# Optimization experiments

Measured on AMD Instinct MI355X. Metric: run time of the kernel, lower is better.

The kernel has to match this reference:

```python
import jax, jax.numpy as jnp
import numpy as np

NUM_GROUPS = 32
EPS = 1e-6
NUM_HEADS = 8


def group_norm32(x, gamma, beta):
    # GroupNorm32: compute in float32, cast back to input dtype.
    b, c, h, w = x.shape
    xf = x.astype(jnp.float32).reshape(b, NUM_GROUPS, -1)  # [b, G, (C/G)*h*w]
    mean = xf.mean(axis=-1, keepdims=True)
    var = xf.var(axis=-1, keepdims=True)
    xn = ((xf - mean) * jax.lax.rsqrt(var + EPS)).reshape(b, c, h, w)
    xn = xn * gamma[None, :, None, None] + beta[None, :, None, None]
    return xn.astype(x.dtype)


def setup_inputs() -> dict:
    key = jax.random.key(0)
    ks = jax.random.split(key, 4)
    b, c, h, w = 16, 512, 32, 32
    x = jax.random.normal(ks[0], (b, c, h, w), dtype=jnp.float32)
    w_qkv = jax.random.normal(ks[1], (3 * c, c), dtype=jnp.float32) * (1.0 / np.sqrt(c))
    b_qkv = jnp.zeros((3 * c,), dtype=jnp.float32)
    w_proj = jax.random.normal(ks[2], (c, c), dtype=jnp.float32) * (1.0 / np.sqrt(c))
    b_proj = jnp.zeros((c,), dtype=jnp.float32)
    gamma = jnp.ones((c,), dtype=jnp.float32)
    beta = jnp.zeros((c,), dtype=jnp.float32)
    return {"x": x, "w_qkv": w_qkv, "b_qkv": b_qkv, "w_proj": w_proj,
            "b_proj": b_proj, "gamma": gamma, "beta": beta}


def reference(x, w_qkv, b_qkv, w_proj, b_proj, gamma, beta):
    b, c, h, w = x.shape
    H = NUM_HEADS
    d = c // H
    n = h * w
    x_norm = group_norm32(x, gamma, beta)
    # 1x1 conv == channel matmul
    qkv = jnp.einsum('oc,bchw->bohw', w_qkv, x_norm) + b_qkv[None, :, None, None]
    q, k, v = jnp.split(qkv, 3, axis=1)
    q = q.reshape(b, H, d, n)
    k = k.reshape(b, H, d, n)
    v = v.reshape(b, H, d, n)
    scale = d ** (-0.5)
    attn = jnp.einsum('bhdn,bhdm->bhnm', q, k) * scale  # [b,H,n,n]
    attn = jax.nn.softmax(attn, axis=-1)
    out = jnp.einsum('bhnm,bhdm->bhdn', attn, v).reshape(b, c, h, w)
    proj = jnp.einsum('oc,bchw->bohw', w_proj, out) + b_proj[None, :, None, None]
    return x + proj
```

## Files before the change

### kernel.cpp

```cpp
#include <hip/hip_runtime.h>
#include <hip/hip_bf16.h>

typedef __bf16 bf16;
typedef __bf16 bf16x4 __attribute__((ext_vector_type(4)));
typedef __bf16 bf16x8 __attribute__((ext_vector_type(8)));
typedef float  floatx4 __attribute__((ext_vector_type(4)));
typedef float  f32x16  __attribute__((ext_vector_type(16)));

#define BB   16
#define CC   512
#define NN   1024
#define GG   32
#define CPG  16
#define HH   8
#define DD   64
#define QSCALE 0.18033688011f

#if __has_builtin(__builtin_amdgcn_exp2f)
#define EXP2(x) __builtin_amdgcn_exp2f(x)
#else
#define EXP2(x) exp2f(x)
#endif

__device__ inline floatx4 mfma16(bf16x8 a, bf16x8 b, floatx4 c) {
    return __builtin_amdgcn_mfma_f32_16x16x32_bf16(a, b, c, 0, 0, 0);
}
__device__ inline f32x16 mfma32(bf16x8 a, bf16x8 b, f32x16 c) {
    return __builtin_amdgcn_mfma_f32_32x32x16_bf16(a, b, c, 0, 0, 0);
}

__device__ inline floatx4 zero4() {
    floatx4 z; z[0] = 0.f; z[1] = 0.f; z[2] = 0.f; z[3] = 0.f; return z;
}

__device__ inline void gl_lds16(const bf16* g, bf16* l) {
    __builtin_amdgcn_global_load_lds(
        (const __attribute__((address_space(1))) unsigned int*)g,
        (__attribute__((address_space(3))) unsigned int*)l, 16, 0, 0);
}

__device__ inline unsigned cvt_pk_bf16(float a, float b) {
    unsigned r;
    asm("v_cvt_pk_bf16_f32 %0, %1, %2" : "=v"(r) : "v"(a), "v"(b));
    return r;
}
__device__ inline void pl32swap(unsigned &x, unsigned &y) {
    asm volatile("v_permlane32_swap_b32 %0, %1" : "+v"(x), "+v"(y));
}

__device__ inline float ldf(const void* p, size_t i, int isb) {
    return isb ? (float)((const bf16*)p)[i] : ((const float*)p)[i];
}
__device__ inline floatx4 ldf4(const void* p, size_t i, int isb) {
    floatx4 o;
    if (isb) {
        bf16x4 v = *(const bf16x4*)((const bf16*)p + i);
        #pragma unroll
        for (int j = 0; j < 4; ++j) o[j] = (float)v[j];
    } else {
        o = *(const floatx4*)((const float*)p + i);
    }
    return o;
}
__device__ inline void stf(void* p, size_t i, float v, int isb) {
    if (isb) ((bf16*)p)[i] = (bf16)v; else ((float*)p)[i] = v;
}

__global__ __launch_bounds__(256) void flag_kernel(const void* x, const void* wq,
        const void* wp, const void* gamma, int* flags) {
    __shared__ int bad[3];
    const int tid = threadIdx.x;
    if (tid < 3) bad[tid] = 0;
    __syncthreads();
    const void* arrs[3] = {x, wq, wp};
    #pragma unroll
    for (int a = 0; a < 3; ++a) {
        const unsigned short* u = (const unsigned short*)arrs[a];
        int c = 0;
        for (int i = tid * 32; i < tid * 32 + 32; ++i) {
            if ((u[i] & 0x7F80) == 0x7F80) c = 1;
        }
        if (c) atomicOr(&bad[a], 1);
    }
    __syncthreads();
    if (tid == 0) {
        flags[0] = bad[0] ? 0 : 1;
        flags[1] = bad[1] ? 0 : 1;
        flags[2] = bad[2] ? 0 : 1;
        flags[3] = (((const unsigned short*)gamma)[0] == 0x3F80) ? 1 : 0;
    }
}

__global__ __launch_bounds__(256) void cvt_kernel(const void* __restrict__ src,
        bf16* __restrict__ dst, int n, const int* __restrict__ flags, int fidx) {
    const int f = flags[fidx];
    int i = (blockIdx.x * 256 + threadIdx.x) * 4;
    if (i >= n) return;
    if (f) {
        *(bf16x4*)(dst + i) = *(const bf16x4*)((const bf16*)src + i);
    } else {
        const float* s = (const float*)src + i;
        bf16x4 o;
        #pragma unroll
        for (int j = 0; j < 4; ++j) o[j] = (bf16)s[j];
        *(bf16x4*)(dst + i) = o;
    }
}

__global__ __launch_bounds__(256) void gn_kernel(const void* __restrict__ x,
        const void* __restrict__ gamma, const void* __restrict__ beta,
        bf16* __restrict__ xn_t, const int* __restrict__ flags, int b0) {
    const int fx = flags[0], fg = flags[3];
    const int bg = blockIdx.x;
    const int bl = bg >> 5, g = bg & 31;
    const int tid = threadIdx.x;
    const size_t xbase = (size_t)((b0 + bl) * CC + g * CPG) * NN;

    float s = 0.f, ss = 0.f;
    for (int i = tid * 4; i < CPG * NN; i += 1024) {
        floatx4 v = ldf4(x, xbase + i, fx);
        #pragma unroll
        for (int j = 0; j < 4; ++j) { s += v[j]; ss += v[j] * v[j]; }
    }
    for (int off = 32; off > 0; off >>= 1) {
        s  += __shfl_down(s, off);
        ss += __shfl_down(ss, off);
    }
    __shared__ float red[8];
    __shared__ float stats[2];
    const int wave = tid >> 6;
    if ((tid & 63) == 0) { red[wave] = s; red[4 + wave] = ss; }
    __syncthreads();
    if (tid == 0) {
        float S  = red[0] + red[1] + red[2] + red[3];
        float SS = red[4] + red[5] + red[6] + red[7];
        float mean = S * (1.0f / (CPG * NN));
        float var  = SS * (1.0f / (CPG * NN)) - mean * mean;
        stats[0] = mean;
        stats[1] = rsqrtf(fmaxf(var, 0.f) + 1e-6f);
    }
    __syncthreads();
    const float mean = stats[0], rstd = stats[1];

    __shared__ __align__(16) float tile[CPG][64];
    const int cn = tid >> 4;
    const int nb = (tid & 15) * 4;
    const float gm1 = ldf(gamma, g * CPG + cn, fg);
    const float bt1 = ldf(beta,  g * CPG + cn, fg);
    const int n2 = tid >> 2, cq = tid & 3;
    for (int nt = 0; nt < NN / 64; ++nt) {
        floatx4 v = ldf4(x, xbase + (size_t)cn * NN + nt * 64 + nb, fx);
        #pragma unroll
        for (int j = 0; j < 4; ++j)
            tile[cn][nb + j] = (v[j] - mean) * rstd * gm1 + bt1;
        __syncthreads();
        bf16x4 o;
        #pragma unroll
        for (int k = 0; k < 4; ++k) o[k] = (bf16)tile[cq * 4 + k][n2];
        *(bf16x4*)(xn_t + (size_t)(bl * NN + nt * 64 + n2) * CC + g * CPG + cq * 4) = o;
        __syncthreads();
    }
}

__global__ __launch_bounds__(256) void qkv_kernel(const bf16* __restrict__ wq_b,
        const bf16* __restrict__ b_qkv, const bf16* __restrict__ xn_t,
        bf16* __restrict__ q_t, bf16* __restrict__ k_pk, bf16* __restrict__ v_pk) {
    __shared__ __align__(16) bf16 As[2][128 * 32];
    __shared__ __align__(16) bf16 Bs[2][128 * 32];

    const int ntile = blockIdx.x;
    const int mtile = blockIdx.y;
    const int bl = blockIdx.z;
    const int w = threadIdx.x >> 6, lane = threadIdx.x & 63;
    const int l16 = lane & 15, quad = lane >> 4;
    const int wr = w >> 1, wc = w & 1;

    const int mbase = mtile * 128, nbase = ntile * 128;
    const int srow = lane >> 2;
    const int scol = (((lane & 3) ^ ((srow >> 1) & 3)) << 3);
    const bf16* Ag = wq_b + (size_t)(mbase + w * 32 + srow) * CC + scol;
    const bf16* Bg = xn_t + (size_t)bl * NN * CC + (size_t)(nbase + w * 32 + srow) * CC + scol;
    const int ldso = (2 * w) * 512;

#define QSTAGE(buf, k0) do {                                  \
    gl_lds16(Ag + (k0),           &As[buf][ldso]);            \
    gl_lds16(Ag + 16 * CC + (k0), &As[buf][ldso + 512]);      \
    gl_lds16(Bg + (k0),           &Bs[buf][ldso]);            \
    gl_lds16(Bg + 16 * CC + (k0), &Bs[buf][ldso + 512]);      \
} while (0)

    floatx4 acc[4][4];
    #pragma unroll
    for (int i = 0; i < 4; ++i)
        #pragma unroll
        for (int j = 0; j < 4; ++j) acc[i][j] = zero4();

    const int sw = (l16 >> 1) & 3;
    QSTAGE(0, 0);

    for (int it = 0; it < 16; ++it) {
        const int cur = it & 1;
        const int nk = ((it + 1) & 15) * 32;
        QSTAGE(cur ^ 1, nk);
        asm volatile("s_waitcnt vmcnt(4)" ::: "memory");
        __builtin_amdgcn_s_barrier();

        bf16x8 af[4], bfr[4];
        #pragma unroll
        for (int mt = 0; mt < 4; ++mt)
            af[mt] = *(const bf16x8*)&As[cur][(wr * 64 + mt * 16 + l16) * 32 + ((quad ^ sw) << 3)];
        #pragma unroll
        for (int nt = 0; nt < 4; ++nt)
            bfr[nt] = *(const bf16x8*)&Bs[cur][(wc * 64 + nt * 16 + l16) * 32 + ((quad ^ sw) << 3)];

        asm volatile("s_waitcnt lgkmcnt(0)" ::: "memory");
        __builtin_amdgcn_s_barrier();

        #pragma unroll
        for (int mt = 0; mt < 4; ++mt)
            #pragma unroll
            for (int nt = 0; nt < 4; ++nt)
                acc[mt][nt] = mfma16(af[mt], bfr[nt], acc[mt][nt]);
    }
#undef QSTAGE

    const int qsel = mtile >> 2;
    const int obase = (mtile & 3) * 128;
    #pragma unroll
    for (int mt = 0; mt < 4; ++mt) {
        const int op = obase + wr * 64 + mt * 16 + quad * 4;
        float bias[4];
        #pragma unroll
        for (int r = 0; r < 4; ++r) bias[r] = (float)b_qkv[qsel * CC + op + r];
        #pragma unroll
        for (int nt = 0; nt < 4; ++nt) {
            const int p = nbase + wc * 64 + nt * 16 + l16;
            if (qsel == 0) {
                int h = op >> 6, d0 = op & 63;
                bf16x4 o;
                #pragma unroll
                for (int r = 0; r < 4; ++r) o[r] = (bf16)((acc[mt][nt][r] + bias[r]) * QSCALE);
                *(bf16x4*)(q_t + ((size_t)(bl * HH + h) * NN + p) * DD + d0) = o;
            } else if (qsel == 1) {
                int h = op >> 6, d0 = op & 63;
                bf16x4 o;
                #pragma unroll
                for (int r = 0; r < 4; ++r) o[r] = (bf16)(acc[mt][nt][r] + bias[r]);
                size_t off = ((size_t)(bl * HH + h) << 16) + ((size_t)(p >> 5) << 11)
                           + ((d0 >> 4) << 9) + (((d0 >> 3) & 1) << 8)
                           + ((p & 31) << 3) + (d0 & 7);
                *(bf16x4*)(k_pk + off) = o;
            } else {
                #pragma unroll
                for (int r = 0; r < 4; ++r) {
                    int c = op + r;
                    int h = c >> 6, d = c & 63;
                    size_t off = ((size_t)(bl * HH + h) << 16) + ((size_t)(p >> 4) << 10)
                               + ((d >> 5) << 9) + (((p >> 3) & 1) << 8)
                               + ((d & 31) << 3) + (p & 7);
                    v_pk[off] = (bf16)(acc[mt][nt][r] + bias[r]);
                }
            }
        }
    }
}

__global__ __launch_bounds__(256) void attn_kernel(const bf16* __restrict__ q_t,
        const bf16* __restrict__ k_pk, const bf16* __restrict__ v_pk,
        bf16* __restrict__ attn_out) {
    const int lid = blockIdx.x + (blockIdx.y << 2);
    const int xcd = lid & 7, jj = lid >> 3;
    const int bh = xcd * (gridDim.y >> 3) + (jj >> 2);
    const int qb = jj & 3;
    const int bl = bh >> 3, h = bh & 7;
    const int tid = threadIdx.x;
    const int w = tid >> 6, lane = tid & 63;
    const int l31 = lane & 31, hi = lane >> 5;

    const bf16* kpb = k_pk + ((size_t)bh << 16) + (hi << 8) + (l31 << 3);
    const bf16* vpb = v_pk + ((size_t)bh << 16) + (hi << 8) + (l31 << 3);

    const int qbase = qb * 256 + w * 64;
    const bf16* qp = q_t + ((size_t)bh * NN + qbase + l31) * DD + hi * 8;
    bf16x8 qf0[4], qf1[4];
    #pragma unroll
    for (int ks = 0; ks < 4; ++ks) {
        qf0[ks] = *(const bf16x8*)(qp + ks * 16);
        qf1[ks] = *(const bf16x8*)(qp + (size_t)32 * DD + ks * 16);
    }

    f32x16 oacc0[2], oacc1[2];
    #pragma unroll
    for (int i = 0; i < 2; ++i)
        #pragma unroll
        for (int r = 0; r < 16; ++r) { oacc0[i][r] = 0.f; oacc1[i][r] = 0.f; }
    float lrun0 = 0.f, lrun1 = 0.f;

#define EXPPACK(SV, PW, LR) do {                                          \
    float p[16];                                                          \
    _Pragma("unroll")                                                     \
    for (int r = 0; r < 16; ++r) { p[r] = EXP2((SV)[r]); LR += p[r]; }    \
    _Pragma("unroll")                                                     \
    for (int i = 0; i < 8; ++i) PW[i] = cvt_pk_bf16(p[2*i], p[2*i+1]);    \
    pl32swap(PW[0], PW[2]); pl32swap(PW[1], PW[3]);                       \
    pl32swap(PW[4], PW[6]); pl32swap(PW[5], PW[7]);                       \
} while (0)

    bf16x8 kf[4];
    #pragma unroll
    for (int ks = 0; ks < 4; ++ks)
        kf[ks] = *(const bf16x8*)(kpb + (ks << 9));

    #pragma unroll 2
    for (int kb = 0; kb < 32; ++kb) {
        bf16x8 vfr[4];
        #pragma unroll
        for (int tt = 0; tt < 2; ++tt)
            #pragma unroll
            for (int db = 0; db < 2; ++db)
                vfr[tt * 2 + db] = *(const bf16x8*)(vpb + (size_t)((kb * 2 + tt) << 10) + (db << 9));
        const int kbn = (kb + 1) & 31;
        bf16x8 kfn[4];
        #pragma unroll
        for (int ks = 0; ks < 4; ++ks)
            kfn[ks] = *(const bf16x8*)(kpb + (size_t)(kbn << 11) + (ks << 9));

        f32x16 s0, s1;
        #pragma unroll
        for (int r = 0; r < 16; ++r) { s0[r] = 0.f; s1[r] = 0.f; }
        #pragma unroll
        for (int ks = 0; ks < 4; ++ks) s0 = mfma32(kf[ks], qf0[ks], s0);
        #pragma unroll
        for (int ks = 0; ks < 4; ++ks) s1 = mfma32(kf[ks], qf1[ks], s1);

        unsigned pw0[8], pw1[8];
        EXPPACK(s0, pw0, lrun0);
        EXPPACK(s1, pw1, lrun1);

        #pragma unroll
        for (int tt = 0; tt < 2; ++tt) {
            union { unsigned u[4]; bf16x8 v; } pf0, pf1;
            #pragma unroll
            for (int i = 0; i < 4; ++i) {
                pf0.u[i] = pw0[tt * 4 + i];
                pf1.u[i] = pw1[tt * 4 + i];
            }
            #pragma unroll
            for (int db = 0; db < 2; ++db) {
                bf16x8 vf = vfr[tt * 2 + db];
                oacc0[db] = mfma32(vf, pf0.v, oacc0[db]);
                oacc1[db] = mfma32(vf, pf1.v, oacc1[db]);
            }
        }
        #pragma unroll
        for (int ks = 0; ks < 4; ++ks) kf[ks] = kfn[ks];
    }
#undef EXPPACK

    lrun0 += __shfl_xor(lrun0, 32);
    lrun1 += __shfl_xor(lrun1, 32);
    const float inv0 = 1.0f / lrun0;
    const float inv1 = 1.0f / lrun1;
    bf16* ob0 = attn_out + ((size_t)bl * NN + qbase + l31) * CC + h * DD;
    bf16* ob1 = ob0 + (size_t)32 * CC;
    #pragma unroll
    for (int db = 0; db < 2; ++db) {
        #pragma unroll
        for (int g = 0; g < 4; ++g) {
            bf16x4 o0, o1;
            #pragma unroll
            for (int e = 0; e < 4; ++e) {
                o0[e] = (bf16)(oacc0[db][4 * g + e] * inv0);
                o1[e] = (bf16)(oacc1[db][4 * g + e] * inv1);
            }
            *(bf16x4*)(ob0 + db * 32 + g * 8 + hi * 4) = o0;
            *(bf16x4*)(ob1 + db * 32 + g * 8 + hi * 4) = o1;
        }
    }
}

__global__ __launch_bounds__(256) void proj_kernel(const bf16* __restrict__ wp_b,
        const bf16* __restrict__ b_proj, const bf16* __restrict__ attn_out,
        const void* __restrict__ x, void* __restrict__ out,
        const int* __restrict__ flags, int b0) {
    __shared__ __align__(16) bf16 As[2][128 * 32];
    __shared__ __align__(16) bf16 Bs[2][128 * 32];

    const int fx = flags[0];
    const int ntile = blockIdx.x;
    const int mtile = blockIdx.y;
    const int bl = blockIdx.z;
    const int w = threadIdx.x >> 6, lane = threadIdx.x & 63;
    const int l16 = lane & 15, quad = lane >> 4;
    const int wr = w >> 1, wc = w & 1;

    const int mbase = mtile * 128, nbase = ntile * 128;
    const int srow = lane >> 2;
    const int scol = (((lane & 3) ^ ((srow >> 1) & 3)) << 3);
    const bf16* Ag = wp_b + (size_t)(mbase + w * 32 + srow) * CC + scol;
    const bf16* Bg = attn_out + (size_t)bl * NN * CC + (size_t)(nbase + w * 32 + srow) * CC + scol;
    const int ldso = (2 * w) * 512;

#define PSTAGE(buf, k0) do {                                  \
    gl_lds16(Ag + (k0),           &As[buf][ldso]);            \
    gl_lds16(Ag + 16 * CC + (k0), &As[buf][ldso + 512]);      \
    gl_lds16(Bg + (k0),           &Bs[buf][ldso]);            \
    gl_lds16(Bg + 16 * CC + (k0), &Bs[buf][ldso + 512]);      \
} while (0)

    floatx4 acc[4][4];
    #pragma unroll
    for (int i = 0; i < 4; ++i)
        #pragma unroll
        for (int j = 0; j < 4; ++j) acc[i][j] = zero4();

    const int sw = (l16 >> 1) & 3;
    PSTAGE(0, 0);

    for (int it = 0; it < 16; ++it) {
        const int cur = it & 1;
        const int nk = ((it + 1) & 15) * 32;
        PSTAGE(cur ^ 1, nk);
        asm volatile("s_waitcnt vmcnt(4)" ::: "memory");
        __builtin_amdgcn_s_barrier();

        bf16x8 af[4], bfr[4];
        #pragma unroll
        for (int mt = 0; mt < 4; ++mt)
            af[mt] = *(const bf16x8*)&As[cur][(wr * 64 + mt * 16 + l16) * 32 + ((quad ^ sw) << 3)];
        #pragma unroll
        for (int nt = 0; nt < 4; ++nt)
            bfr[nt] = *(const bf16x8*)&Bs[cur][(wc * 64 + nt * 16 + l16) * 32 + ((quad ^ sw) << 3)];

        asm volatile("s_waitcnt lgkmcnt(0)" ::: "memory");
        __builtin_amdgcn_s_barrier();

        #pragma unroll
        for (int mt = 0; mt < 4; ++mt)
            #pragma unroll
            for (int nt = 0; nt < 4; ++nt)
                acc[mt][nt] = mfma16(af[mt], bfr[nt], acc[mt][nt]);
    }
#undef PSTAGE

    #pragma unroll
    for (int mt = 0; mt < 4; ++mt) {
        const int op = mbase + wr * 64 + mt * 16 + quad * 4;
        float bias[4];
        #pragma unroll
        for (int r = 0; r < 4; ++r) bias[r] = (float)b_proj[op + r];
        #pragma unroll
        for (int nt = 0; nt < 4; ++nt) {
            const int p = nbase + wc * 64 + nt * 16 + l16;
            #pragma unroll
            for (int r = 0; r < 4; ++r) {
                size_t idx = ((size_t)(b0 + bl) * CC + op + r) * NN + p;
                float xv = ldf(x, idx, fx);
                stf(out, idx, xv + acc[mt][nt][r] + bias[r], fx);
            }
        }
    }
}

extern "C" void kernel_launch(void* const* d_in, const int* in_sizes, int n_in,
                              void* d_out, int out_size, void* d_ws, size_t ws_size,
                              hipStream_t stream) {
    const void* x      = d_in[0];
    const void* w_qkv  = d_in[1];
    const bf16* b_qkv  = (const bf16*)d_in[2];
    const void* w_proj = d_in[3];
    const bf16* b_proj = (const bf16*)d_in[4];
    const void* gamma  = d_in[5];
    const void* beta   = d_in[6];

    const size_t MB = (size_t)1 << 20;
    const int NQKV = 3 * CC * CC;
    const int NPRJ = CC * CC;
    const size_t wbytes = (size_t)(NQKV + NPRJ) * sizeof(bf16) + 4096;
    int bc = 0;
    for (int c = 16; c >= 1; c >>= 1) {
        if ((size_t)c * 4 * MB + wbytes <= ws_size) { bc = c; break; }
    }
    if (bc == 0) {
        hipMemsetAsync(d_out, 0, (size_t)out_size * sizeof(bf16), stream);
        return;
    }

    const size_t cs = (size_t)bc * MB;
    char* ws = (char*)d_ws;
    bf16* xn_t = (bf16*)(ws);
    bf16* q_t  = (bf16*)(ws + cs);
    bf16* k_pk = (bf16*)(ws + 2 * cs);
    bf16* v_pk = (bf16*)(ws + 3 * cs);
    int*  flags = (int*)(ws + 4 * cs);
    bf16* wq_b = (bf16*)(ws + 4 * cs + 4096);
    bf16* wp_b = wq_b + NQKV;
    bf16* attn_out = xn_t;

    flag_kernel<<<1, 256, 0, stream>>>(x, w_qkv, w_proj, gamma, flags);
    cvt_kernel<<<NQKV / 1024, 256, 0, stream>>>(w_qkv, wq_b, NQKV, flags, 1);
    cvt_kernel<<<NPRJ / 1024, 256, 0, stream>>>(w_proj, wp_b, NPRJ, flags, 2);

    for (int b0 = 0; b0 < BB; b0 += bc) {
        gn_kernel<<<dim3(bc * GG), 256, 0, stream>>>(x, gamma, beta, xn_t, flags, b0);
        qkv_kernel<<<dim3(8, 12, bc), 256, 0, stream>>>(wq_b, b_qkv, xn_t, q_t, k_pk, v_pk);
        attn_kernel<<<dim3(4, bc * HH), 256, 0, stream>>>(q_t, k_pk, v_pk, attn_out);
        proj_kernel<<<dim3(8, 4, bc), 256, 0, stream>>>(wp_b, b_proj, attn_out, x, d_out, flags, b0);
    }
}
```

Measured before the change: 235.3 us.

## Halve per-wave query tile in attention to raise occupancy, add setprio

Each wave in the attention kernel now processes 32 query rows instead of 64. The grid is doubled to 8 query blocks per head, with the XCD-aware block remapping adjusted to match. K fragments are loaded inside the loop instead of being prefetched a step ahead, launch bounds request 4 blocks per CU, and s_setprio brackets the MFMA sections. This cuts register pressure so more waves can be resident, but each K/V fragment loaded is reused for half as many queries, which doubles K/V traffic from cache.

```diff
diff --git a/kernel.cpp b/kernel.cpp
--- a/kernel.cpp
+++ b/kernel.cpp
@@ -265,13 +265,14 @@
     }
 }
 
-__global__ __launch_bounds__(256) void attn_kernel(const bf16* __restrict__ q_t,
+__global__ __launch_bounds__(256, 4) void attn_kernel(const bf16* __restrict__ q_t,
         const bf16* __restrict__ k_pk, const bf16* __restrict__ v_pk,
         bf16* __restrict__ attn_out) {
-    const int lid = blockIdx.x + (blockIdx.y << 2);
+    const int lid = blockIdx.x + (blockIdx.y << 3);
     const int xcd = lid & 7, jj = lid >> 3;
-    const int bh = xcd * (gridDim.y >> 3) + (jj >> 2);
-    const int qb = jj & 3;
+    const int hpx = gridDim.y >> 3;
+    const int bh = xcd * hpx + (jj >> 3);
+    const int qb = jj & 7;
     const int bl = bh >> 3, h = bh & 7;
     const int tid = threadIdx.x;
     const int w = tid >> 6, lane = tid & 63;
@@ -280,101 +281,73 @@
     const bf16* kpb = k_pk + ((size_t)bh << 16) + (hi << 8) + (l31 << 3);
     const bf16* vpb = v_pk + ((size_t)bh << 16) + (hi << 8) + (l31 << 3);
 
-    const int qbase = qb * 256 + w * 64;
+    const int qbase = qb * 128 + w * 32;
     const bf16* qp = q_t + ((size_t)bh * NN + qbase + l31) * DD + hi * 8;
-    bf16x8 qf0[4], qf1[4];
-    #pragma unroll
-    for (int ks = 0; ks < 4; ++ks) {
-        qf0[ks] = *(const bf16x8*)(qp + ks * 16);
-        qf1[ks] = *(const bf16x8*)(qp + (size_t)32 * DD + ks * 16);
-    }
-
-    f32x16 oacc0[2], oacc1[2];
+    bf16x8 qf[4];
+    #pragma unroll
+    for (int ks = 0; ks < 4; ++ks) qf[ks] = *(const bf16x8*)(qp + ks * 16);
+
+    f32x16 oacc[2];
     #pragma unroll
     for (int i = 0; i < 2; ++i)
         #pragma unroll
-        for (int r = 0; r < 16; ++r) { oacc0[i][r] = 0.f; oacc1[i][r] = 0.f; }
-    float lrun0 = 0.f, lrun1 = 0.f;
-
-#define EXPPACK(SV, PW, LR) do {                                          \
-    float p[16];                                                          \
-    _Pragma("unroll")                                                     \
-    for (int r = 0; r < 16; ++r) { p[r] = EXP2((SV)[r]); LR += p[r]; }    \
-    _Pragma("unroll")                                                     \
-    for (int i = 0; i < 8; ++i) PW[i] = cvt_pk_bf16(p[2*i], p[2*i+1]);    \
-    pl32swap(PW[0], PW[2]); pl32swap(PW[1], PW[3]);                       \
-    pl32swap(PW[4], PW[6]); pl32swap(PW[5], PW[7]);                       \
-} while (0)
-
-    bf16x8 kf[4];
-    #pragma unroll
-    for (int ks = 0; ks < 4; ++ks)
-        kf[ks] = *(const bf16x8*)(kpb + (ks << 9));
+        for (int r = 0; r < 16; ++r) oacc[i][r] = 0.f;
+    float lrun = 0.f;
 
     #pragma unroll 2
     for (int kb = 0; kb < 32; ++kb) {
+        bf16x8 kf[4];
+        #pragma unroll
+        for (int ks = 0; ks < 4; ++ks)
+            kf[ks] = *(const bf16x8*)(kpb + (size_t)(kb << 11) + (ks << 9));
         bf16x8 vfr[4];
         #pragma unroll
         for (int tt = 0; tt < 2; ++tt)
             #pragma unroll
             for (int db = 0; db < 2; ++db)
                 vfr[tt * 2 + db] = *(const bf16x8*)(vpb + (size_t)((kb * 2 + tt) << 10) + (db << 9));
-        const int kbn = (kb + 1) & 31;
-        bf16x8 kfn[4];
-        #pragma unroll
-        for (int ks = 0; ks < 4; ++ks)
-            kfn[ks] = *(const bf16x8*)(kpb + (size_t)(kbn << 11) + (ks << 9));
-
-        f32x16 s0, s1;
-        #pragma unroll
-        for (int r = 0; r < 16; ++r) { s0[r] = 0.f; s1[r] = 0.f; }
-        #pragma unroll
-        for (int ks = 0; ks < 4; ++ks) s0 = mfma32(kf[ks], qf0[ks], s0);
-        #pragma unroll
-        for (int ks = 0; ks < 4; ++ks) s1 = mfma32(kf[ks], qf1[ks], s1);
-
-        unsigned pw0[8], pw1[8];
-        EXPPACK(s0, pw0, lrun0);
-        EXPPACK(s1, pw1, lrun1);
-
+
+        f32x16 s;
+        #pragma unroll
+        for (int r = 0; r < 16; ++r) s[r] = 0.f;
+        __builtin_amdgcn_s_setprio(1);
+        #pragma unroll
+        for (int ks = 0; ks < 4; ++ks) s = mfma32(kf[ks], qf[ks], s);
+        __builtin_amdgcn_s_setprio(0);
+
+        float p[16];
+        #pragma unroll
+        for (int r = 0; r < 16; ++r) { p[r] = EXP2(s[r]); lrun += p[r]; }
+        unsigned pw[8];
+        #pragma unroll
+        for (int i = 0; i < 8; ++i) pw[i] = cvt_pk_bf16(p[2 * i], p[2 * i + 1]);
+        pl32swap(pw[0], pw[2]); pl32swap(pw[1], pw[3]);
+        pl32swap(pw[4], pw[6]); pl32swap(pw[5], pw[7]);
+
+        __builtin_amdgcn_s_setprio(1);
         #pragma unroll
         for (int tt = 0; tt < 2; ++tt) {
-            union { unsigned u[4]; bf16x8 v; } pf0, pf1;
-            #pragma unroll
-            for (int i = 0; i < 4; ++i) {
-                pf0.u[i] = pw0[tt * 4 + i];
-                pf1.u[i] = pw1[tt * 4 + i];
-            }
-            #pragma unroll
-            for (int db = 0; db < 2; ++db) {
-                bf16x8 vf = vfr[tt * 2 + db];
-                oacc0[db] = mfma32(vf, pf0.v, oacc0[db]);
-                oacc1[db] = mfma32(vf, pf1.v, oacc1[db]);
-            }
+            union { unsigned u[4]; bf16x8 v; } pf;
+            pf.u[0] = pw[tt * 4 + 0]; pf.u[1] = pw[tt * 4 + 1];
+            pf.u[2] = pw[tt * 4 + 2]; pf.u[3] = pw[tt * 4 + 3];
+            #pragma unroll
+            for (int db = 0; db < 2; ++db)
+                oacc[db] = mfma32(vfr[tt * 2 + db], pf.v, oacc[db]);
         }
-        #pragma unroll
-        for (int ks = 0; ks < 4; ++ks) kf[ks] = kfn[ks];
-    }
-#undef EXPPACK
-
-    lrun0 += __shfl_xor(lrun0, 32);
-    lrun1 += __shfl_xor(lrun1, 32);
-    const float inv0 = 1.0f / lrun0;
-    const float inv1 = 1.0f / lrun1;
-    bf16* ob0 = attn_out + ((size_t)bl * NN + qbase + l31) * CC + h * DD;
-    bf16* ob1 = ob0 + (size_t)32 * CC;
+        __builtin_amdgcn_s_setprio(0);
+    }
+
+    lrun += __shfl_xor(lrun, 32);
+    const float inv = 1.0f / lrun;
+    bf16* ob = attn_out + ((size_t)bl * NN + qbase + l31) * CC + h * DD;
     #pragma unroll
     for (int db = 0; db < 2; ++db) {
         #pragma unroll
         for (int g = 0; g < 4; ++g) {
-            bf16x4 o0, o1;
-            #pragma unroll
-            for (int e = 0; e < 4; ++e) {
-                o0[e] = (bf16)(oacc0[db][4 * g + e] * inv0);
-                o1[e] = (bf16)(oacc1[db][4 * g + e] * inv1);
-            }
-            *(bf16x4*)(ob0 + db * 32 + g * 8 + hi * 4) = o0;
-            *(bf16x4*)(ob1 + db * 32 + g * 8 + hi * 4) = o1;
+            bf16x4 o;
+            #pragma unroll
+            for (int e = 0; e < 4; ++e) o[e] = (bf16)(oacc[db][4 * g + e] * inv);
+            *(bf16x4*)(ob + db * 32 + g * 8 + hi * 4) = o;
         }
     }
 }
@@ -504,7 +477,7 @@
     for (int b0 = 0; b0 < BB; b0 += bc) {
         gn_kernel<<<dim3(bc * GG), 256, 0, stream>>>(x, gamma, beta, xn_t, flags, b0);
         qkv_kernel<<<dim3(8, 12, bc), 256, 0, stream>>>(wq_b, b_qkv, xn_t, q_t, k_pk, v_pk);
-        attn_kernel<<<dim3(4, bc * HH), 256, 0, stream>>>(q_t, k_pk, v_pk, attn_out);
+        attn_kernel<<<dim3(8, bc * HH), 256, 0, stream>>>(q_t, k_pk, v_pk, attn_out);
         proj_kernel<<<dim3(8, 4, bc), 256, 0, stream>>>(wp_b, b_proj, attn_out, x, d_out, flags, b0);
     }
 }
```

Measured after the change: 238.4 us. About the same (+1.3%).

## Split attention key range across two wave halves and merge via LDS

Applied to the files above, without the earlier changes.

Doubles the attention block to 512 threads, with each group of four waves handling half of the key blocks for the same queries. The partial outputs and row sums are combined through shared memory after a barrier. It also drops the software prefetch of the next K tile and wraps the MFMA sections in s_setprio. This raises the number of waves per CU to hide latency, at the cost of 64KB of LDS, an extra reduction step, and no explicit K prefetch.

```diff
diff --git a/kernel.cpp b/kernel.cpp
--- a/kernel.cpp
+++ b/kernel.cpp
@@ -265,22 +265,24 @@
     }
 }
 
-__global__ __launch_bounds__(256) void attn_kernel(const bf16* __restrict__ q_t,
+__global__ __launch_bounds__(512, 4) void attn_kernel(const bf16* __restrict__ q_t,
         const bf16* __restrict__ k_pk, const bf16* __restrict__ v_pk,
         bf16* __restrict__ attn_out) {
     const int lid = blockIdx.x + (blockIdx.y << 2);
     const int xcd = lid & 7, jj = lid >> 3;
-    const int bh = xcd * (gridDim.y >> 3) + (jj >> 2);
+    const int hpx = gridDim.y >> 3;
+    const int bh = xcd * hpx + (jj >> 2);
     const int qb = jj & 3;
     const int bl = bh >> 3, h = bh & 7;
     const int tid = threadIdx.x;
     const int w = tid >> 6, lane = tid & 63;
+    const int qg = w & 3, half = w >> 2;
     const int l31 = lane & 31, hi = lane >> 5;
 
     const bf16* kpb = k_pk + ((size_t)bh << 16) + (hi << 8) + (l31 << 3);
     const bf16* vpb = v_pk + ((size_t)bh << 16) + (hi << 8) + (l31 << 3);
 
-    const int qbase = qb * 256 + w * 64;
+    const int qbase = qb * 256 + qg * 64;
     const bf16* qp = q_t + ((size_t)bh * NN + qbase + l31) * DD + hi * 8;
     bf16x8 qf0[4], qf1[4];
     #pragma unroll
@@ -306,37 +308,35 @@
     pl32swap(PW[4], PW[6]); pl32swap(PW[5], PW[7]);                       \
 } while (0)
 
-    bf16x8 kf[4];
-    #pragma unroll
-    for (int ks = 0; ks < 4; ++ks)
-        kf[ks] = *(const bf16x8*)(kpb + (ks << 9));
-
+    const int kb0 = half << 4;
     #pragma unroll 2
-    for (int kb = 0; kb < 32; ++kb) {
+    for (int kb = kb0; kb < kb0 + 16; ++kb) {
+        bf16x8 kf[4];
+        #pragma unroll
+        for (int ks = 0; ks < 4; ++ks)
+            kf[ks] = *(const bf16x8*)(kpb + (size_t)(kb << 11) + (ks << 9));
         bf16x8 vfr[4];
         #pragma unroll
         for (int tt = 0; tt < 2; ++tt)
             #pragma unroll
             for (int db = 0; db < 2; ++db)
                 vfr[tt * 2 + db] = *(const bf16x8*)(vpb + (size_t)((kb * 2 + tt) << 10) + (db << 9));
-        const int kbn = (kb + 1) & 31;
-        bf16x8 kfn[4];
-        #pragma unroll
-        for (int ks = 0; ks < 4; ++ks)
-            kfn[ks] = *(const bf16x8*)(kpb + (size_t)(kbn << 11) + (ks << 9));
 
         f32x16 s0, s1;
         #pragma unroll
         for (int r = 0; r < 16; ++r) { s0[r] = 0.f; s1[r] = 0.f; }
+        __builtin_amdgcn_s_setprio(1);
         #pragma unroll
         for (int ks = 0; ks < 4; ++ks) s0 = mfma32(kf[ks], qf0[ks], s0);
         #pragma unroll
         for (int ks = 0; ks < 4; ++ks) s1 = mfma32(kf[ks], qf1[ks], s1);
+        __builtin_amdgcn_s_setprio(0);
 
         unsigned pw0[8], pw1[8];
         EXPPACK(s0, pw0, lrun0);
         EXPPACK(s1, pw1, lrun1);
 
+        __builtin_amdgcn_s_setprio(1);
         #pragma unroll
         for (int tt = 0; tt < 2; ++tt) {
             union { unsigned u[4]; bf16x8 v; } pf0, pf1;
@@ -347,15 +347,42 @@
             }
             #pragma unroll
             for (int db = 0; db < 2; ++db) {
-                bf16x8 vf = vfr[tt * 2 + db];
-                oacc0[db] = mfma32(vf, pf0.v, oacc0[db]);
-                oacc1[db] = mfma32(vf, pf1.v, oacc1[db]);
+                oacc0[db] = mfma32(vfr[tt * 2 + db], pf0.v, oacc0[db]);
+                oacc1[db] = mfma32(vfr[tt * 2 + db], pf1.v, oacc1[db]);
             }
         }
-        #pragma unroll
-        for (int ks = 0; ks < 4; ++ks) kf[ks] = kfn[ks];
+        __builtin_amdgcn_s_setprio(0);
     }
 #undef EXPPACK
+
+    __shared__ __align__(16) floatx4 Osh[4][16][64];
+    __shared__ float Lsh[4][2][64];
+
+    if (half == 1) {
+        #pragma unroll
+        for (int c = 0; c < 16; ++c) {
+            const f32x16 &src = (c < 4) ? oacc0[0] : (c < 8) ? oacc0[1]
+                              : (c < 12) ? oacc1[0] : oacc1[1];
+            floatx4 t;
+            #pragma unroll
+            for (int e = 0; e < 4; ++e) t[e] = src[(c & 3) * 4 + e];
+            Osh[qg][c][lane] = t;
+        }
+        Lsh[qg][0][lane] = lrun0;
+        Lsh[qg][1][lane] = lrun1;
+    }
+    __syncthreads();
+    if (half == 1) return;
+    #pragma unroll
+    for (int c = 0; c < 16; ++c) {
+        f32x16 &dst = (c < 4) ? oacc0[0] : (c < 8) ? oacc0[1]
+                    : (c < 12) ? oacc1[0] : oacc1[1];
+        floatx4 t = Osh[qg][c][lane];
+        #pragma unroll
+        for (int e = 0; e < 4; ++e) dst[(c & 3) * 4 + e] += t[e];
+    }
+    lrun0 += Lsh[qg][0][lane];
+    lrun1 += Lsh[qg][1][lane];
 
     lrun0 += __shfl_xor(lrun0, 32);
     lrun1 += __shfl_xor(lrun1, 32);
@@ -504,7 +531,7 @@
     for (int b0 = 0; b0 < BB; b0 += bc) {
         gn_kernel<<<dim3(bc * GG), 256, 0, stream>>>(x, gamma, beta, xn_t, flags, b0);
         qkv_kernel<<<dim3(8, 12, bc), 256, 0, stream>>>(wq_b, b_qkv, xn_t, q_t, k_pk, v_pk);
-        attn_kernel<<<dim3(4, bc * HH), 256, 0, stream>>>(q_t, k_pk, v_pk, attn_out);
+        attn_kernel<<<dim3(4, bc * HH), 512, 0, stream>>>(q_t, k_pk, v_pk, attn_out);
         proj_kernel<<<dim3(8, 4, bc), 256, 0, stream>>>(wp_b, b_proj, attn_out, x, d_out, flags, b0);
     }
 }
```

Measured after the change: 449.4 us. 1.91x slower.

## Software-pipeline QK^T one block ahead of softmax and PV in attention

Applied to the files above, without the earlier changes.

The attention loop now computes the QK^T scores for the next key block at the end of each iteration, after the PV MFMAs, so the exp/pack of the current block can overlap with matrix work from neighbouring iterations. A prologue computes the first block's scores before the loop, and s_setprio raises wave priority around the MFMA section. The last iteration computes one redundant wrapped-around score block. Keeping two score accumulators live across iterations raises register pressure, and the loop is no longer unrolled by 2.

```diff
diff --git a/kernel.cpp b/kernel.cpp
--- a/kernel.cpp
+++ b/kernel.cpp
@@ -270,7 +270,8 @@
         bf16* __restrict__ attn_out) {
     const int lid = blockIdx.x + (blockIdx.y << 2);
     const int xcd = lid & 7, jj = lid >> 3;
-    const int bh = xcd * (gridDim.y >> 3) + (jj >> 2);
+    const int hpx = gridDim.y >> 3;
+    const int bh = xcd * hpx + (jj >> 2);
     const int qb = jj & 3;
     const int bl = bh >> 3, h = bh & 7;
     const int tid = threadIdx.x;
@@ -306,37 +307,38 @@
     pl32swap(PW[4], PW[6]); pl32swap(PW[5], PW[7]);                       \
 } while (0)
 
-    bf16x8 kf[4];
-    #pragma unroll
-    for (int ks = 0; ks < 4; ++ks)
-        kf[ks] = *(const bf16x8*)(kpb + (ks << 9));
-
-    #pragma unroll 2
+    f32x16 s0p, s1p;
+    #pragma unroll
+    for (int r = 0; r < 16; ++r) { s0p[r] = 0.f; s1p[r] = 0.f; }
+    {
+        bf16x8 kf[4];
+        #pragma unroll
+        for (int ks = 0; ks < 4; ++ks)
+            kf[ks] = *(const bf16x8*)(kpb + (ks << 9));
+        #pragma unroll
+        for (int ks = 0; ks < 4; ++ks) s0p = mfma32(kf[ks], qf0[ks], s0p);
+        #pragma unroll
+        for (int ks = 0; ks < 4; ++ks) s1p = mfma32(kf[ks], qf1[ks], s1p);
+    }
+
     for (int kb = 0; kb < 32; ++kb) {
+        const int kbn = (kb + 1) & 31;
+        bf16x8 kfn[4];
+        #pragma unroll
+        for (int ks = 0; ks < 4; ++ks)
+            kfn[ks] = *(const bf16x8*)(kpb + (size_t)(kbn << 11) + (ks << 9));
         bf16x8 vfr[4];
         #pragma unroll
         for (int tt = 0; tt < 2; ++tt)
             #pragma unroll
             for (int db = 0; db < 2; ++db)
                 vfr[tt * 2 + db] = *(const bf16x8*)(vpb + (size_t)((kb * 2 + tt) << 10) + (db << 9));
-        const int kbn = (kb + 1) & 31;
-        bf16x8 kfn[4];
-        #pragma unroll
-        for (int ks = 0; ks < 4; ++ks)
-            kfn[ks] = *(const bf16x8*)(kpb + (size_t)(kbn << 11) + (ks << 9));
-
-        f32x16 s0, s1;
-        #pragma unroll
-        for (int r = 0; r < 16; ++r) { s0[r] = 0.f; s1[r] = 0.f; }
-        #pragma unroll
-        for (int ks = 0; ks < 4; ++ks) s0 = mfma32(kf[ks], qf0[ks], s0);
-        #pragma unroll
-        for (int ks = 0; ks < 4; ++ks) s1 = mfma32(kf[ks], qf1[ks], s1);
 
         unsigned pw0[8], pw1[8];
-        EXPPACK(s0, pw0, lrun0);
-        EXPPACK(s1, pw1, lrun1);
-
+        EXPPACK(s0p, pw0, lrun0);
+        EXPPACK(s1p, pw1, lrun1);
+
+        __builtin_amdgcn_s_setprio(1);
         #pragma unroll
         for (int tt = 0; tt < 2; ++tt) {
             union { unsigned u[4]; bf16x8 v; } pf0, pf1;
@@ -347,13 +349,18 @@
             }
             #pragma unroll
             for (int db = 0; db < 2; ++db) {
-                bf16x8 vf = vfr[tt * 2 + db];
-                oacc0[db] = mfma32(vf, pf0.v, oacc0[db]);
-                oacc1[db] = mfma32(vf, pf1.v, oacc1[db]);
+                oacc0[db] = mfma32(vfr[tt * 2 + db], pf0.v, oacc0[db]);
+                oacc1[db] = mfma32(vfr[tt * 2 + db], pf1.v, oacc1[db]);
             }
         }
-        #pragma unroll
-        for (int ks = 0; ks < 4; ++ks) kf[ks] = kfn[ks];
+
+        #pragma unroll
+        for (int r = 0; r < 16; ++r) { s0p[r] = 0.f; s1p[r] = 0.f; }
+        #pragma unroll
+        for (int ks = 0; ks < 4; ++ks) s0p = mfma32(kfn[ks], qf0[ks], s0p);
+        #pragma unroll
+        for (int ks = 0; ks < 4; ++ks) s1p = mfma32(kfn[ks], qf1[ks], s1p);
+        __builtin_amdgcn_s_setprio(0);
     }
 #undef EXPPACK
 
```

New measurement: 238.5 us. Within noise of the previous version (+1.4%).
